# Performance work log

Measured on AMD Instinct MI355X. Metric: run time of the kernel, lower is better.

The kernel has to match this reference:

```python
import jax, jax.numpy as jnp
import numpy as np

C = 4096
C8 = C // 8  # 512, must equal h*w
B, H, W = 32, 16, 32


def setup_inputs() -> dict:
    key = jax.random.key(0)
    ks = jax.random.split(key, 8)
    s = 0.02
    return {
        "x": jax.random.normal(ks[0], (B, C, H, W), dtype=jnp.float32),
        "Wq": jax.random.normal(ks[1], (C8, C), dtype=jnp.float32) * s,
        "bq": jax.random.normal(ks[2], (C8,), dtype=jnp.float32) * s,
        "Wk": jax.random.normal(ks[3], (C8, C), dtype=jnp.float32) * s,
        "bk": jax.random.normal(ks[4], (C8,), dtype=jnp.float32) * s,
        "Wv": jax.random.normal(ks[5], (C, C), dtype=jnp.float32) * s,
        "bv": jax.random.normal(ks[6], (C,), dtype=jnp.float32) * s,
        "gamma": jax.random.normal(ks[7], (1,), dtype=jnp.float32),
    }


def reference(x, Wq, bq, Wk, bk, Wv, bv, gamma):
    b, c, h, w = x.shape
    xf = x.reshape(b, c, h * w)               # (b, c, hw)
    # 1x1 conv == per-position linear over channels
    q = jnp.einsum("oc,bcl->bol", Wq, xf) + bq[None, :, None]   # (b, c8, hw)
    k = jnp.einsum("oc,bcl->bol", Wk, xf) + bk[None, :, None]   # (b, c8, hw)
    v = jnp.einsum("oc,bcl->bol", Wv, xf) + bv[None, :, None]   # (b, c, hw)
    # energy = bmm(Q, K^T): (b, c8, c8); no sqrt(d) scaling (faithful)
    energy = jnp.einsum("bol,bpl->bop", q, k)
    attn = jax.nn.softmax(energy, axis=-1)
    # out = bmm(V, attn^T): out[b,c,p] = sum_k V[b,c,k] * attn[b,p,k]
    out = jnp.einsum("bck,bpk->bcp", v, attn)  # requires hw == c8
    out = out.reshape(b, c, h, w)
    return gamma * out + x
```

## Files before the change

### kernel.cpp

```cpp
#include <hip/hip_runtime.h>


typedef _Float16 f16;
typedef _Float16 h8 __attribute__((ext_vector_type(8)));
typedef _Float16 h4 __attribute__((ext_vector_type(4)));
typedef float fx4 __attribute__((ext_vector_type(4)));

#define CC  4096
#define C8  512
#define HWD 512
#define NB  32


__device__ __forceinline__ h8 ldfragC(const char* s, int row, int cb) {
  const int b = ((row << 7) | cb) ^ ((row & 7) << 4);
  return *reinterpret_cast<const h8*>(s + b);
}

#define AS1C(p) ((const __attribute__((address_space(1))) unsigned int*)(p))
#define AS3(p)  ((__attribute__((address_space(3))) unsigned int*)(p))

#define STAGE(bufsel) { \
  char* la_ = smem + ((bufsel) << 16); \
  char* lb_ = la_ + 32768; \
  _Pragma("unroll") for (int q = 0; q < 4; ++q) { \
    __builtin_amdgcn_global_load_lds(AS1C(pA[q]), AS3(la_ + (q << 13) + w1024), 16, 0, 0); \
    __builtin_amdgcn_global_load_lds(AS1C(pB[q]), AS3(lb_ + (q << 13) + w1024), 16, 0, 0); \
    pA[q] += 128; pB[q] += 128; } }

#define LOADA(hm) { \
  _Pragma("unroll") for (int f = 0; f < 4; ++f) \
  _Pragma("unroll") for (int ks = 0; ks < 2; ++ks) \
    a[f][ks] = ldfragC(At, wr * 128 + (hm) * 64 + f * 16 + frow, ks * 64 + kq); }

#define LOADB(hn) { \
  _Pragma("unroll") for (int g = 0; g < 2; ++g) \
  _Pragma("unroll") for (int ks = 0; ks < 2; ++ks) \
    b[g][ks] = ldfragC(Bt, wc * 64 + (hn) * 32 + g * 16 + frow, ks * 64 + kq); }

#define MMA(hm, hn) { \
  __builtin_amdgcn_s_setprio(1); \
  _Pragma("unroll") for (int f = 0; f < 4; ++f) \
  _Pragma("unroll") for (int g = 0; g < 2; ++g) \
  _Pragma("unroll") for (int ks = 0; ks < 2; ++ks) \
    acc[(hm) * 4 + f][(hn) * 2 + g] = __builtin_amdgcn_mfma_f32_16x16x32_f16( \
        a[f][ks], b[g][ks], acc[(hm) * 4 + f][(hn) * 2 + g], 0, 0, 0); \
  __builtin_amdgcn_s_setprio(0); }

template<int EPI>
__global__ __launch_bounds__(512, 2) void gemm256(
    const f16* __restrict__ Ah, const f16* __restrict__ Bh,
    int lda, int ldb, long sAb, long sBb, long sCb, int ldc, int K,
    const float* __restrict__ bias, float* __restrict__ Cf, f16* __restrict__ Ch,
    const float* __restrict__ resid, const float* __restrict__ gam)
{
  extern __shared__ __align__(16) char smem[];
  const int F  = blockIdx.x;
  const int Vv = ((F & 7) << 7) | (F >> 3);
  const int bz = Vv >> 5;
  const int m0 = (Vv & 15) << 8;
  const int n0 = ((Vv >> 4) & 1) << 8;

  const int T = threadIdx.x;
  const int lane = T & 63;
  const int w = T >> 6;
  const int wr = w >> 2, wc = w & 3;
  const int frow = lane & 15;
  const int kq = (lane >> 4) << 4;
  const int w1024 = w << 10;

  const int rr = T >> 3;
  const int corig = ((T & 7) << 4) ^ ((rr & 7) << 4);
  const char* pA[4];
  const char* pB[4];
#pragma unroll
  for (int q = 0; q < 4; ++q) {
    pA[q] = (const char*)(Ah + bz * sAb + (long)(m0 + q * 64 + rr) * lda) + corig;
    pB[q] = (const char*)(Bh + bz * sBb + (long)(n0 + q * 64 + rr) * ldb) + corig;
  }

  fx4 acc[8][4] = {};
  const int nt = K >> 6;

  STAGE(0)
  for (int t = 0; t < nt; ++t) {
    if (t + 1 < nt) {
      STAGE((t + 1) & 1)
      asm volatile("s_waitcnt vmcnt(8)" ::: "memory");
    } else {
      asm volatile("s_waitcnt vmcnt(0)" ::: "memory");
    }
    asm volatile("s_barrier" ::: "memory");
    const char* At = smem + ((t & 1) << 16);
    const char* Bt = At + 32768;
    h8 a[4][2], b[2][2];
    LOADA(0) LOADB(0) MMA(0, 0)
    LOADA(1)          MMA(1, 0)
              LOADB(1) MMA(1, 1)
    LOADA(0)          MMA(0, 1)
    __builtin_amdgcn_sched_barrier(0);
    asm volatile("s_waitcnt lgkmcnt(0)" ::: "memory");
    asm volatile("s_barrier" ::: "memory");
  }

  const int cm = (lane >> 4) << 2;
  const int cn = lane & 15;
  const float g0 = (EPI == 3) ? gam[0] : 0.f;
#pragma unroll
  for (int fm = 0; fm < 8; ++fm) {
    const int gr0 = m0 + wr * 128 + fm * 16 + cm;
#pragma unroll
    for (int fn = 0; fn < 4; ++fn) {
      const int gc = n0 + wc * 64 + fn * 16 + cn;
#pragma unroll
      for (int j = 0; j < 4; ++j) {
        const long ci = bz * sCb + (long)(gr0 + j) * ldc + gc;
        if constexpr (EPI == 1) Ch[ci] = (f16)(acc[fm][fn][j] + bias[gr0 + j]);
        else                    Cf[ci] = g0 * acc[fm][fn][j] + resid[ci];
      }
    }
  }
}

__device__ __forceinline__ void stage_tile(const f16* __restrict__ g, f16* __restrict__ s, int ld) {
  const int t = threadIdx.x;
#pragma unroll
  for (int i = 0; i < 4; ++i) {
    const int id = t + i * 256;
    const int r = id >> 3, j = id & 7;
    const uint4 v = *reinterpret_cast<const uint4*>(g + (long)r * ld + (j << 3));
    char* p = reinterpret_cast<char*>(s);
    const int b = ((r << 7) + (j << 4)) ^ ((r & 7) << 4);
    *reinterpret_cast<uint4*>(p + b) = v;
  }
}

__device__ __forceinline__ h8 ldfrag(const f16* s, int row, int kb) {
  const int b = ((row << 7) + kb) ^ ((row & 7) << 4);
  return *reinterpret_cast<const h8*>(reinterpret_cast<const char*>(s) + b);
}

template<int EPI>
__global__ __launch_bounds__(256) void gemm_tri(
    const f16* __restrict__ Ah, const f16* __restrict__ Al,
    const f16* __restrict__ Bh, const f16* __restrict__ Bl,
    int K, int lda, int ldb, long sAb, long sBb, long sCb, int ldc,
    const float* __restrict__ bias,
    float* __restrict__ Cf, f16* __restrict__ Ch, f16* __restrict__ Cl)
{
  constexpr int TILE = 128 * 64;
  __shared__ __align__(16) f16 smem[4 * TILE];
  f16* sAh = smem;
  f16* sBh = smem + TILE;
  f16* sAl = smem + 2 * TILE;
  f16* sBl = smem + 3 * TILE;

  const int bz = blockIdx.z;
  const int m0 = blockIdx.y * 128, n0 = blockIdx.x * 128;
  const f16* gA = Ah + (long)bz * sAb + (long)m0 * lda;
  const f16* gB = Bh + (long)bz * sBb + (long)n0 * ldb;

  const int lane = threadIdx.x & 63;
  const int wid  = threadIdx.x >> 6;
  const int wr = wid >> 1, wc = wid & 1;
  const int frow = lane & 15;
  const int kq = (lane >> 4) << 4;

  fx4 acc[4][4] = {};

  for (int k0 = 0; k0 < K; k0 += 64) {
    stage_tile(gA + k0, sAh, lda);
    stage_tile(gB + k0, sBh, ldb);
    stage_tile(Al + (long)bz * sAb + (long)m0 * lda + k0, sAl, lda);
    stage_tile(Bl + (long)bz * sBb + (long)n0 * ldb + k0, sBl, ldb);
    __syncthreads();
#pragma unroll
    for (int ks = 0; ks < 2; ++ks) {
      const int kb = ks * 64 + kq;
      h8 aH[4], bH[4], aL[4], bL[4];
#pragma unroll
      for (int f = 0; f < 4; ++f) {
        aH[f] = ldfrag(sAh, wr * 64 + f * 16 + frow, kb);
        bH[f] = ldfrag(sBh, wc * 64 + f * 16 + frow, kb);
        aL[f] = ldfrag(sAl, wr * 64 + f * 16 + frow, kb);
        bL[f] = ldfrag(sBl, wc * 64 + f * 16 + frow, kb);
      }
#pragma unroll
      for (int fm = 0; fm < 4; ++fm)
#pragma unroll
        for (int fn = 0; fn < 4; ++fn) {
          acc[fm][fn] = __builtin_amdgcn_mfma_f32_16x16x32_f16(aH[fm], bH[fn], acc[fm][fn], 0, 0, 0);
          acc[fm][fn] = __builtin_amdgcn_mfma_f32_16x16x32_f16(aH[fm], bL[fn], acc[fm][fn], 0, 0, 0);
          acc[fm][fn] = __builtin_amdgcn_mfma_f32_16x16x32_f16(aL[fm], bH[fn], acc[fm][fn], 0, 0, 0);
        }
    }
    __syncthreads();
  }

  const int cm = (lane >> 4) * 4;
  const int cn = lane & 15;
#pragma unroll
  for (int fm = 0; fm < 4; ++fm) {
    const int gr0 = m0 + wr * 64 + fm * 16 + cm;
#pragma unroll
    for (int fn = 0; fn < 4; ++fn) {
      const int gc = n0 + wc * 64 + fn * 16 + cn;
#pragma unroll
      for (int j = 0; j < 4; ++j) {
        const int gr = gr0 + j;
        const long ci = (long)bz * sCb + (long)gr * ldc + gc;
        float v = acc[fm][fn][j];
        if constexpr (EPI == 0) {
          v += bias[gr];
          const f16 h = (f16)v;
          Ch[ci] = h;
          Cl[ci] = (f16)(v - (float)h);
        } else {
          Cf[ci] = v;
        }
      }
    }
  }
}

__global__ void transpose_split_k(const float* __restrict__ x, f16* __restrict__ xh, f16* __restrict__ xl) {
  __shared__ float t[32][33];
  const int l0 = blockIdx.x * 32, c0 = blockIdx.y * 32;
  const long bi = (long)blockIdx.z * CC * HWD;
  const long bo = (long)blockIdx.z * HWD * CC;
  const int tx = threadIdx.x, ty = threadIdx.y;
#pragma unroll
  for (int i = 0; i < 32; i += 8)
    t[ty + i][tx] = x[bi + (long)(c0 + ty + i) * HWD + l0 + tx];
  __syncthreads();
#pragma unroll
  for (int i = 0; i < 32; i += 8) {
    const float v = t[tx][ty + i];
    const f16 h = (f16)v;
    const long o = bo + (long)(l0 + ty + i) * CC + c0 + tx;
    xh[o] = h;
    xl[o] = (f16)(v - (float)h);
  }
}

template<bool HASLO>
__global__ void split_k(const float* __restrict__ in, f16* __restrict__ hi, f16* __restrict__ lo, long n) {
  const long i = ((long)blockIdx.x * blockDim.x + threadIdx.x) * 4;
  if (i >= n) return;
  const float4 v = *reinterpret_cast<const float4*>(in + i);
  const float vv[4] = {v.x, v.y, v.z, v.w};
  h4 h, l;
#pragma unroll
  for (int j = 0; j < 4; ++j) {
    const f16 hh = (f16)vv[j];
    h[j] = hh;
    l[j] = (f16)(vv[j] - (float)hh);
  }
  *reinterpret_cast<h4*>(hi + i) = h;
  if constexpr (HASLO) *reinterpret_cast<h4*>(lo + i) = l;
}

__global__ __launch_bounds__(256) void softmax_k(const float* __restrict__ E, f16* __restrict__ attn) {
  const int lane = threadIdx.x & 63;
  const int wid  = threadIdx.x >> 6;
  const long row = (long)blockIdx.x * 4 + wid;
  const float* e = E + row * 512;
  const float4 a = *reinterpret_cast<const float4*>(e + lane * 8);
  const float4 b = *reinterpret_cast<const float4*>(e + lane * 8 + 4);
  float vv[8] = {a.x, a.y, a.z, a.w, b.x, b.y, b.z, b.w};
  float m = vv[0];
#pragma unroll
  for (int i = 1; i < 8; ++i) m = fmaxf(m, vv[i]);
#pragma unroll
  for (int s = 32; s > 0; s >>= 1) m = fmaxf(m, __shfl_xor(m, s));
  float sum = 0.f;
  float ex[8];
#pragma unroll
  for (int i = 0; i < 8; ++i) { ex[i] = __expf(vv[i] - m); sum += ex[i]; }
#pragma unroll
  for (int s = 32; s > 0; s >>= 1) sum += __shfl_xor(sum, s);
  const float inv = 1.f / sum;
  h8 o;
#pragma unroll
  for (int i = 0; i < 8; ++i) o[i] = (f16)(ex[i] * inv);
  *reinterpret_cast<h8*>(attn + row * 512 + lane * 8) = o;
}

extern "C" void kernel_launch(void* const* d_in, const int* in_sizes, int n_in,
                              void* d_out, int out_size, void* d_ws, size_t ws_size,
                              hipStream_t stream) {
  const float* x  = (const float*)d_in[0];
  const float* Wq = (const float*)d_in[1];
  const float* bq = (const float*)d_in[2];
  const float* Wk = (const float*)d_in[3];
  const float* bk = (const float*)d_in[4];
  const float* Wv = (const float*)d_in[5];
  const float* bv = (const float*)d_in[6];
  const float* gm = (const float*)d_in[7];
  float* out = (float*)d_out;

  const size_t szXT = (size_t)NB * HWD * CC;
  const size_t szQK = (size_t)NB * C8 * HWD;
  const size_t szW  = (size_t)C8 * CC;
  const size_t szWv = (size_t)CC * CC;
  const size_t needBytes = (2 * szXT + 4 * szQK + 4 * szW + szWv) * sizeof(f16);
  if (ws_size < needBytes) return;

  f16* xT_h = (f16*)d_ws;
  f16* xT_l = xT_h + szXT;
  f16* v16  = xT_l;
  f16* q_h  = xT_h + 2 * szXT;
  f16* q_l  = q_h + szQK;
  f16* k_h  = q_l + szQK;
  f16* k_l  = k_h + szQK;
  f16* wq_h = k_l + szQK;
  f16* wq_l = wq_h + szW;
  f16* wk_h = wq_l + szW;
  f16* wk_l = wk_h + szW;
  f16* attn = wq_h;
  f16* wv_h = wk_l + szW;
  float* E  = (float*)wv_h;

  split_k<true ><<<dim3((C8 * CC) / 1024), 256, 0, stream>>>(Wq, wq_h, wq_l, (long)C8 * CC);
  split_k<true ><<<dim3((C8 * CC) / 1024), 256, 0, stream>>>(Wk, wk_h, wk_l, (long)C8 * CC);
  split_k<false><<<dim3((CC * CC) / 1024), 256, 0, stream>>>(Wv, wv_h, nullptr, (long)CC * CC);
  transpose_split_k<<<dim3(HWD / 32, CC / 32, NB), dim3(32, 8), 0, stream>>>(x, xT_h, xT_l);
  gemm_tri<0><<<dim3(4, 4, NB), 256, 0, stream>>>(wq_h, wq_l, xT_h, xT_l, CC, CC, CC,
      0L, (long)HWD * CC, (long)C8 * HWD, HWD, bq, nullptr, q_h, q_l);
  gemm_tri<0><<<dim3(4, 4, NB), 256, 0, stream>>>(wk_h, wk_l, xT_h, xT_l, CC, CC, CC,
      0L, (long)HWD * CC, (long)C8 * HWD, HWD, bk, nullptr, k_h, k_l);
  gemm256<1><<<dim3(1024), 512, 131072, stream>>>(wv_h, xT_h, CC, CC,
      0L, (long)HWD * CC, (long)CC * HWD, HWD, CC, bv, nullptr, v16, nullptr, nullptr);
  gemm_tri<2><<<dim3(4, 4, NB), 256, 0, stream>>>(q_h, q_l, k_h, k_l, HWD, HWD, HWD,
      (long)C8 * HWD, (long)C8 * HWD, (long)C8 * C8, C8, nullptr, E, nullptr, nullptr);
  softmax_k<<<dim3(NB * C8 / 4), 256, 0, stream>>>(E, attn);
  gemm256<3><<<dim3(1024), 512, 131072, stream>>>(v16, attn, HWD, HWD,
      (long)CC * HWD, (long)C8 * HWD, (long)CC * HWD, HWD, C8, nullptr, out, nullptr, x, gm);
}
```

Before: 1.369 ms.

## Restructure GEMM inner loop into barrier-synchronized k-half phases

Splits each 64-wide K tile into two k-halves and four phases. Each phase loads A and B fragments, waits on LDS, does a full 4x4 MFMA block and closes with workgroup barriers so waves stay in lockstep (ping-pong style). Fragment registers shrink, which frees VGPRs. The cost is several extra s_barriers per tile and less overlap between LDS reads and MFMA work.

```diff
diff --git a/kernel.cpp b/kernel.cpp
--- a/kernel.cpp
+++ b/kernel.cpp
@@ -28,24 +28,25 @@
     __builtin_amdgcn_global_load_lds(AS1C(pB[q]), AS3(lb_ + (q << 13) + w1024), 16, 0, 0); \
     pA[q] += 128; pB[q] += 128; } }
 
-#define LOADA(hm) { \
+#define LOADA(hm, kh) { \
   _Pragma("unroll") for (int f = 0; f < 4; ++f) \
-  _Pragma("unroll") for (int ks = 0; ks < 2; ++ks) \
-    a[f][ks] = ldfragC(At, wr * 128 + (hm) * 64 + f * 16 + frow, ks * 64 + kq); }
-
-#define LOADB(hn) { \
-  _Pragma("unroll") for (int g = 0; g < 2; ++g) \
-  _Pragma("unroll") for (int ks = 0; ks < 2; ++ks) \
-    b[g][ks] = ldfragC(Bt, wc * 64 + (hn) * 32 + g * 16 + frow, ks * 64 + kq); }
-
-#define MMA(hm, hn) { \
+    a[f] = ldfragC(At, wr * 128 + (hm) * 64 + f * 16 + frow, (kh) * 64 + kq); }
+
+#define LOADB(kh) { \
+  _Pragma("unroll") for (int g = 0; g < 4; ++g) \
+    b[g] = ldfragC(Bt, wc * 64 + g * 16 + frow, (kh) * 64 + kq); }
+
+#define PHASE(hm) { \
+  asm volatile("s_barrier" ::: "memory"); \
+  asm volatile("s_waitcnt lgkmcnt(0)" ::: "memory"); \
+  __builtin_amdgcn_sched_barrier(0); \
   __builtin_amdgcn_s_setprio(1); \
   _Pragma("unroll") for (int f = 0; f < 4; ++f) \
-  _Pragma("unroll") for (int g = 0; g < 2; ++g) \
-  _Pragma("unroll") for (int ks = 0; ks < 2; ++ks) \
-    acc[(hm) * 4 + f][(hn) * 2 + g] = __builtin_amdgcn_mfma_f32_16x16x32_f16( \
-        a[f][ks], b[g][ks], acc[(hm) * 4 + f][(hn) * 2 + g], 0, 0, 0); \
-  __builtin_amdgcn_s_setprio(0); }
+  _Pragma("unroll") for (int g = 0; g < 4; ++g) \
+    acc[(hm) * 4 + f][g] = __builtin_amdgcn_mfma_f32_16x16x32_f16( \
+        a[f], b[g], acc[(hm) * 4 + f][g], 0, 0, 0); \
+  __builtin_amdgcn_s_setprio(0); \
+  asm volatile("s_barrier" ::: "memory"); }
 
 template<int EPI>
 __global__ __launch_bounds__(512, 2) void gemm256(
@@ -84,23 +85,25 @@
 
   STAGE(0)
   for (int t = 0; t < nt; ++t) {
+    const int cur = t & 1;
     if (t + 1 < nt) {
-      STAGE((t + 1) & 1)
+      STAGE(cur ^ 1)
       asm volatile("s_waitcnt vmcnt(8)" ::: "memory");
     } else {
       asm volatile("s_waitcnt vmcnt(0)" ::: "memory");
     }
     asm volatile("s_barrier" ::: "memory");
-    const char* At = smem + ((t & 1) << 16);
+    const char* At = smem + (cur << 16);
     const char* Bt = At + 32768;
-    h8 a[4][2], b[2][2];
-    LOADA(0) LOADB(0) MMA(0, 0)
-    LOADA(1)          MMA(1, 0)
-              LOADB(1) MMA(1, 1)
-    LOADA(0)          MMA(0, 1)
-    __builtin_amdgcn_sched_barrier(0);
-    asm volatile("s_waitcnt lgkmcnt(0)" ::: "memory");
-    asm volatile("s_barrier" ::: "memory");
+    h8 a[4], b[4];
+    LOADA(0, 0) LOADB(0)
+    PHASE(0)
+    LOADA(1, 0)
+    PHASE(1)
+    LOADA(0, 1) LOADB(1)
+    PHASE(0)
+    LOADA(1, 1)
+    PHASE(1)
   }
 
   const int cm = (lane >> 4) << 2;
```

Result: no change. 1.384 ms (+1.1%).

## Restructure 256x256 GEMM main loop into quadrant-staged pipelined K-tiles

Applied to the files above, without the earlier changes.

Splits each 64-deep K tile into four 128-row half-tiles of A and B. Global-to-LDS loads for the next tile are issued in pieces interleaved with the four MMA quadrants, each guarded by partial vmcnt waits and barriers. Warp ownership of the output changes from one contiguous 128x64 region to four strided 64x32 sub-blocks, so the B fragments are reused across the two A halves. The intent is to overlap memory traffic with MFMA work more finely. The cost is more barriers per K tile and reliance on a hand-tuned wait-count ordering.

```diff
diff --git a/kernel.cpp b/kernel.cpp
--- a/kernel.cpp
+++ b/kernel.cpp
@@ -20,32 +20,68 @@
 #define AS1C(p) ((const __attribute__((address_space(1))) unsigned int*)(p))
 #define AS3(p)  ((__attribute__((address_space(3))) unsigned int*)(p))
 
-#define STAGE(bufsel) { \
-  char* la_ = smem + ((bufsel) << 16); \
-  char* lb_ = la_ + 32768; \
-  _Pragma("unroll") for (int q = 0; q < 4; ++q) { \
-    __builtin_amdgcn_global_load_lds(AS1C(pA[q]), AS3(la_ + (q << 13) + w1024), 16, 0, 0); \
-    __builtin_amdgcn_global_load_lds(AS1C(pB[q]), AS3(lb_ + (q << 13) + w1024), 16, 0, 0); \
-    pA[q] += 128; pB[q] += 128; } }
-
-#define LOADA(hm) { \
+#define STG(bufx, h) { \
+  char* hb_ = smem + ((bufx) << 16) + ((h) << 14); \
+  __builtin_amdgcn_global_load_lds(AS1C(pp[(h) * 2 + 0]), AS3(hb_ + (T << 4)), 16, 0, 0); \
+  __builtin_amdgcn_global_load_lds(AS1C(pp[(h) * 2 + 1]), AS3(hb_ + 8192 + (T << 4)), 16, 0, 0); \
+  pp[(h) * 2 + 0] += 128; pp[(h) * 2 + 1] += 128; }
+
+#define READ_A(base) { \
   _Pragma("unroll") for (int f = 0; f < 4; ++f) \
-  _Pragma("unroll") for (int ks = 0; ks < 2; ++ks) \
-    a[f][ks] = ldfragC(At, wr * 128 + (hm) * 64 + f * 16 + frow, ks * 64 + kq); }
-
-#define LOADB(hn) { \
+  _Pragma("unroll") for (int kh = 0; kh < 2; ++kh) \
+    a[f][kh] = ldfragC(base, wr * 64 + f * 16 + frow, kh * 64 + kq); }
+
+#define READ_B(dst, base) { \
   _Pragma("unroll") for (int g = 0; g < 2; ++g) \
-  _Pragma("unroll") for (int ks = 0; ks < 2; ++ks) \
-    b[g][ks] = ldfragC(Bt, wc * 64 + (hn) * 32 + g * 16 + frow, ks * 64 + kq); }
-
-#define MMA(hm, hn) { \
+  _Pragma("unroll") for (int kh = 0; kh < 2; ++kh) \
+    dst[g][kh] = ldfragC(base, wc * 32 + g * 16 + frow, kh * 64 + kq); }
+
+#define MMA(mq, nq, bv) { \
   __builtin_amdgcn_s_setprio(1); \
   _Pragma("unroll") for (int f = 0; f < 4; ++f) \
   _Pragma("unroll") for (int g = 0; g < 2; ++g) \
-  _Pragma("unroll") for (int ks = 0; ks < 2; ++ks) \
-    acc[(hm) * 4 + f][(hn) * 2 + g] = __builtin_amdgcn_mfma_f32_16x16x32_f16( \
-        a[f][ks], b[g][ks], acc[(hm) * 4 + f][(hn) * 2 + g], 0, 0, 0); \
+  _Pragma("unroll") for (int kh = 0; kh < 2; ++kh) \
+    acc[mq][nq][f][g] = __builtin_amdgcn_mfma_f32_16x16x32_f16( \
+        a[f][kh], bv[g][kh], acc[mq][nq][f][g], 0, 0, 0); \
   __builtin_amdgcn_s_setprio(0); }
+
+#define KTILE(cur, dost) { \
+  const char* A0b = smem + ((cur) << 16); \
+  const char* A1b = A0b + 16384; \
+  const char* B0b = A0b + 32768; \
+  const char* B1b = A0b + 49152; \
+  const int nx = (cur) ^ 1; \
+   \
+  READ_A(A0b) READ_B(b0, B0b) \
+  if (dost) STG(nx, 0) \
+  __builtin_amdgcn_s_barrier(); \
+  asm volatile("s_waitcnt lgkmcnt(0)"); \
+  MMA(0, 0, b0) \
+  if (dost) { asm volatile("s_waitcnt vmcnt(4)" ::: "memory"); } \
+  else      { asm volatile("s_waitcnt vmcnt(2)" ::: "memory"); } \
+  __builtin_amdgcn_s_barrier(); \
+   \
+  READ_B(b1, B1b) \
+  if (dost) STG(nx, 2) \
+  __builtin_amdgcn_s_barrier(); \
+  asm volatile("s_waitcnt lgkmcnt(0)"); \
+  MMA(0, 1, b1) \
+  if (dost) { asm volatile("s_waitcnt vmcnt(4)" ::: "memory"); } \
+  else      { asm volatile("s_waitcnt vmcnt(0)" ::: "memory"); } \
+  __builtin_amdgcn_s_barrier(); \
+   \
+  READ_A(A1b) \
+  if (dost) STG(nx, 3) \
+  __builtin_amdgcn_s_barrier(); \
+  asm volatile("s_waitcnt lgkmcnt(0)"); \
+  MMA(1, 0, b0) \
+  __builtin_amdgcn_s_barrier(); \
+   \
+  if (dost) STG(nx, 1) \
+  MMA(1, 1, b1) \
+  if (dost) { asm volatile("s_waitcnt vmcnt(4)" ::: "memory"); } \
+  __builtin_amdgcn_s_barrier(); \
+}
 
 template<int EPI>
 __global__ __launch_bounds__(512, 2) void gemm256(
@@ -67,56 +103,48 @@
   const int wr = w >> 2, wc = w & 3;
   const int frow = lane & 15;
   const int kq = (lane >> 4) << 4;
-  const int w1024 = w << 10;
 
   const int rr = T >> 3;
   const int corig = ((T & 7) << 4) ^ ((rr & 7) << 4);
-  const char* pA[4];
-  const char* pB[4];
-#pragma unroll
-  for (int q = 0; q < 4; ++q) {
-    pA[q] = (const char*)(Ah + bz * sAb + (long)(m0 + q * 64 + rr) * lda) + corig;
-    pB[q] = (const char*)(Bh + bz * sBb + (long)(n0 + q * 64 + rr) * ldb) + corig;
-  }
-
-  fx4 acc[8][4] = {};
+  const char* pp[8];
+#pragma unroll
+  for (int mq = 0; mq < 2; ++mq)
+#pragma unroll
+    for (int j = 0; j < 2; ++j) {
+      pp[mq * 2 + j] = (const char*)(Ah + bz * sAb + (long)(m0 + mq * 128 + j * 64 + rr) * lda) + corig;
+      pp[4 + mq * 2 + j] = (const char*)(Bh + bz * sBb + (long)(n0 + mq * 128 + j * 64 + rr) * ldb) + corig;
+    }
+
+  fx4 acc[2][2][4][2] = {};
+  h8 a[4][2], b0[2][2], b1[2][2];
   const int nt = K >> 6;
 
-  STAGE(0)
+  STG(0, 0) STG(0, 2) STG(0, 3) STG(0, 1)
+  asm volatile("s_waitcnt vmcnt(4)" ::: "memory");
+  __builtin_amdgcn_s_barrier();
+
   for (int t = 0; t < nt; ++t) {
-    if (t + 1 < nt) {
-      STAGE((t + 1) & 1)
-      asm volatile("s_waitcnt vmcnt(8)" ::: "memory");
-    } else {
-      asm volatile("s_waitcnt vmcnt(0)" ::: "memory");
-    }
-    asm volatile("s_barrier" ::: "memory");
-    const char* At = smem + ((t & 1) << 16);
-    const char* Bt = At + 32768;
-    h8 a[4][2], b[2][2];
-    LOADA(0) LOADB(0) MMA(0, 0)
-    LOADA(1)          MMA(1, 0)
-              LOADB(1) MMA(1, 1)
-    LOADA(0)          MMA(0, 1)
-    __builtin_amdgcn_sched_barrier(0);
-    asm volatile("s_waitcnt lgkmcnt(0)" ::: "memory");
-    asm volatile("s_barrier" ::: "memory");
+    KTILE(t & 1, t + 1 < nt)
   }
 
   const int cm = (lane >> 4) << 2;
   const int cn = lane & 15;
   const float g0 = (EPI == 3) ? gam[0] : 0.f;
 #pragma unroll
-  for (int fm = 0; fm < 8; ++fm) {
-    const int gr0 = m0 + wr * 128 + fm * 16 + cm;
-#pragma unroll
-    for (int fn = 0; fn < 4; ++fn) {
-      const int gc = n0 + wc * 64 + fn * 16 + cn;
+  for (int mq = 0; mq < 2; ++mq)
+#pragma unroll
+  for (int f = 0; f < 4; ++f) {
+    const int gr0 = m0 + mq * 128 + wr * 64 + f * 16 + cm;
+#pragma unroll
+    for (int nq = 0; nq < 2; ++nq)
+#pragma unroll
+    for (int g = 0; g < 2; ++g) {
+      const int gc = n0 + nq * 128 + wc * 32 + g * 16 + cn;
 #pragma unroll
       for (int j = 0; j < 4; ++j) {
         const long ci = bz * sCb + (long)(gr0 + j) * ldc + gc;
-        if constexpr (EPI == 1) Ch[ci] = (f16)(acc[fm][fn][j] + bias[gr0 + j]);
-        else                    Cf[ci] = g0 * acc[fm][fn][j] + resid[ci];
+        if constexpr (EPI == 1) Ch[ci] = (f16)(acc[mq][nq][f][g][j] + bias[gr0 + j]);
+        else                    Cf[ci] = g0 * acc[mq][nq][f][g][j] + resid[ci];
       }
     }
   }
```

After: 1.352 ms. Within noise of the previous version (-1.2%).
